# Performance work log

Hardware: AMD Instinct MI355X
Metric: run time of the kernel (lower is better)

Reference implementation:

```python
import jax, jax.numpy as jnp
import numpy as np

B, N, ND = 32, 512, 8        # batch, graph_size, node_dim
L, H, D = 4, 8, 512          # layers, heads, embed_dim
DK = D // H                  # key_dim = val_dim = 64
F = 2048                     # feed_forward_hidden
EPS = 1e-5


def setup_inputs() -> dict:
    key = jax.random.key(0)
    ks = jax.random.split(key, 16)
    u = lambda k, shape, s: jax.random.uniform(k, shape, jnp.float32, -s, s)
    x = jax.random.normal(ks[0], (B, N, ND), dtype=jnp.float32)
    mask = jax.random.randint(ks[1], (B, N, N), 0, 2).astype(jnp.int32)  # 1 = masked
    return {
        "x": x,
        "mask": mask,
        # init_embed Linear(node_dim, embed_dim)
        "We": u(ks[2], (ND, D), 1.0 / np.sqrt(ND)),
        "be": u(ks[3], (D,), 1.0 / np.sqrt(ND)),
        # per-head projections, stacked over layers; torch init: uniform(-1/sqrt(last_dim), ...)
        "Wq": u(ks[4], (L, H, D, DK), 1.0 / np.sqrt(DK)),
        "Wk": u(ks[5], (L, H, D, DK), 1.0 / np.sqrt(DK)),
        "Wv": u(ks[6], (L, H, D, DK), 1.0 / np.sqrt(DK)),
        "Wo": u(ks[7], (L, H, DK, D), 1.0 / np.sqrt(D)),
        # BatchNorm1d affine params (torch default: weight=1, bias=0)
        "g1": jnp.ones((L, D), jnp.float32), "bt1": jnp.zeros((L, D), jnp.float32),
        "g2": jnp.ones((L, D), jnp.float32), "bt2": jnp.zeros((L, D), jnp.float32),
        # FFN
        "W1": u(ks[8], (L, D, F), 1.0 / np.sqrt(D)),
        "bf1": u(ks[9], (L, F), 1.0 / np.sqrt(D)),
        "W2": u(ks[10], (L, F, D), 1.0 / np.sqrt(F)),
        "bf2": u(ks[11], (L, D), 1.0 / np.sqrt(F)),
    }


def _batch_norm(h, g, b):
    # BatchNorm1d in training mode over flattened (B*N, D), biased variance
    hf = h.reshape(-1, h.shape[-1])
    mu = hf.mean(axis=0)
    var = hf.var(axis=0)
    return (h - mu) * jax.lax.rsqrt(var + EPS) * g + b


def reference(x, mask, We, be, Wq, Wk, Wv, Wo, g1, bt1, W1, bf1, W2, bf2, g2, bt2):
    m = mask.astype(bool)[None]                      # [1,B,N,N], True = masked
    scale = 1.0 / np.sqrt(Wq.shape[-1])
    h = x @ We + be                                  # [B,N,D]
    for l in range(Wq.shape[0]):
        # hand-rolled per-head MHA (q = h, self-attention)
        Q = jnp.einsum('bnd,hdk->hbnk', h, Wq[l])
        K = jnp.einsum('bnd,hdk->hbnk', h, Wk[l])
        V = jnp.einsum('bnd,hdv->hbnv', h, Wv[l])
        scores = jnp.einsum('hbqk,hbnk->hbqn', Q, K) * scale   # [H,B,N,N]
        scores = jnp.where(m, -jnp.inf, scores)
        attn = jax.nn.softmax(scores, axis=-1)
        attn = jnp.where(m, 0.0, attn)               # second mask-zeroing pass
        heads = jnp.einsum('hbqn,hbnv->hbqv', attn, V)
        out = jnp.einsum('hbqv,hvd->bqd', heads, Wo[l])
        h = _batch_norm(h + out, g1[l], bt1[l])      # residual + BN
        ff = jax.nn.relu(h @ W1[l] + bf1[l]) @ W2[l] + bf2[l]
        h = _batch_norm(h + ff, g2[l], bt2[l])       # residual + BN
    return (h, h.mean(axis=1))
```

## Files before the change

### kernel.cpp

```cpp
#include <hip/hip_runtime.h>
#include <hip/hip_fp16.h>
#include <math.h>

#define BN_ROWS 16384
#define DIM 512
#define FF 2048
#define LAYERS 4
#define NSEQ 512
#define BATCH 32

typedef _Float16 f16;
typedef __attribute__((ext_vector_type(8))) _Float16 f16x8;
typedef __attribute__((ext_vector_type(4))) _Float16 f16x4;
typedef __attribute__((ext_vector_type(4))) float f32x4;
typedef unsigned long long u64;

__device__ __forceinline__ f32x4 mfma_f16(f16x8 a, f16x8 b, f32x4 c) {
    return __builtin_amdgcn_mfma_f32_16x16x32_f16(a, b, c, 0, 0, 0);
}
__device__ __forceinline__ void gload_lds16(const f16* g, f16* l) {
    __builtin_amdgcn_global_load_lds(
        (const __attribute__((address_space(1))) unsigned int*)g,
        (__attribute__((address_space(3))) unsigned int*)l, 16, 0, 0);
}

__global__ __launch_bounds__(256)
void pack_qkv(const float* __restrict__ Wq, const float* __restrict__ Wk,
              const float* __restrict__ Wv, f16* __restrict__ oh) {
    size_t i = (size_t)blockIdx.x * 256 + threadIdx.x;
    int d = i & 511;
    size_t rr = i >> 9;
    int row = (int)(rr % 1536);
    int lay = (int)(rr / 1536);
    int which = row >> 9, hh = (row >> 6) & 7, k = row & 63;
    const float* W = which == 0 ? Wq : which == 1 ? Wk : Wv;
    oh[i] = (f16)W[(((size_t)lay * 8 + hh) * 512 + d) * 64 + k];
}

__global__ __launch_bounds__(256)
void transpose_w(const float* __restrict__ in, f16* __restrict__ oh, int R, int C) {
    size_t i = (size_t)blockIdx.x * 256 + threadIdx.x;
    int r = (int)(i % R);
    size_t t = i / R;
    int c = (int)(t % C);
    int lay = (int)(t / C);
    oh[i] = (f16)in[((size_t)lay * R + r) * C + c];
}

__global__ __launch_bounds__(256)
void pack_mask(const int* __restrict__ mask, u64* __restrict__ pm) {
    int wid = (blockIdx.x * 256 + threadIdx.x) >> 6;
    int lane = threadIdx.x & 63;
    for (int i = 0; i < 64; i++) {
        size_t word = (size_t)wid * 64 + i;
        u64 bal = __ballot(mask[word * 64 + lane] != 0);
        if (lane == 0) pm[word] = bal;
    }
}

__global__ __launch_bounds__(512)
void embed_kernel(const float* __restrict__ x, const float* __restrict__ We,
                  const float* __restrict__ be, float* __restrict__ h,
                  f16* __restrict__ hf) {
    int row = blockIdx.x, d = threadIdx.x;
    const float* xr = x + (size_t)row * 8;
    float acc = be[d];
#pragma unroll
    for (int c = 0; c < 8; c++) acc += xr[c] * We[c * DIM + d];
    size_t idx = (size_t)row * DIM + d;
    h[idx] = acc;
    hf[idx] = (f16)acc;
}

template<int OUT>
__global__ __launch_bounds__(256)
void gemm_f16(const f16* __restrict__ A, const f16* __restrict__ Bt,
              const float* __restrict__ bias,
              void* __restrict__ O0, void* __restrict__ O1, void* __restrict__ O2,
              int M, int N, int K) {
    __shared__ f16 As[4096];
    __shared__ f16 Bs[4096];
    const int gx = gridDim.x;
    const int nwg = gx * gridDim.y;
    const int id = blockIdx.y * gx + blockIdx.x;
    const int chunk = nwg >> 3;
    const int sid = (id & 7) * chunk + (id >> 3);
    const int row0 = (sid / gx) * 128, col0 = (sid % gx) * 128;

    const int tid = threadIdx.x, l = tid & 63, w = tid >> 6;
    const int wr = w >> 1, wc = w & 1;
    const int fr = l & 15, fq = l >> 4;
    const int srow = l >> 2, skg = (l & 3) * 8;

    f32x4 acc[4][4] = {};
    const size_t aoff = (size_t)(row0 + w * 32 + srow) * K + skg;
    const size_t boff = (size_t)(col0 + w * 32 + srow) * K + skg;

    for (int k0 = 0; k0 < K; k0 += 32) {
        __syncthreads();
        gload_lds16(A + aoff + k0,           &As[(w * 2 + 0) * 512]);
        gload_lds16(A + aoff + 16 * K + k0,  &As[(w * 2 + 1) * 512]);
        gload_lds16(Bt + boff + k0,          &Bs[(w * 2 + 0) * 512]);
        gload_lds16(Bt + boff + 16 * K + k0, &Bs[(w * 2 + 1) * 512]);
        __syncthreads();
        f16x8 a[4], b[4];
#pragma unroll
        for (int i = 0; i < 4; i++)
            a[i] = *(const f16x8*)&As[(wr * 64 + i * 16 + fr) * 32 + fq * 8];
#pragma unroll
        for (int j = 0; j < 4; j++)
            b[j] = *(const f16x8*)&Bs[(wc * 64 + j * 16 + fr) * 32 + fq * 8];
#pragma unroll
        for (int i = 0; i < 4; i++)
#pragma unroll
            for (int j = 0; j < 4; j++)
                acc[i][j] = mfma_f16(a[i], b[j], acc[i][j]);
    }

    if (OUT == 1) {
        f16* C = (f16*)O0;
#pragma unroll
        for (int j = 0; j < 4; j++) {
            int gcol = col0 + wc * 64 + j * 16 + fr;
            float bv = bias[gcol];
#pragma unroll
            for (int i = 0; i < 4; i++) {
                int gr = row0 + wr * 64 + i * 16 + fq * 4;
#pragma unroll
                for (int r = 0; r < 4; r++)
                    C[(size_t)(gr + r) * N + gcol] = (f16)fmaxf(acc[i][j][r] + bv, 0.f);
            }
        }
    } else if (OUT == 2) {
        f16* Qo = (f16*)O0; f16* Ko = (f16*)O1; f16* Vo = (f16*)O2;
#pragma unroll
        for (int j = 0; j < 4; j++) {
            int gcol = col0 + wc * 64 + j * 16 + fr;
            if (gcol < 1024) {
                f16* dst = gcol < 512 ? Qo : Ko;
                int cc = gcol & 511;
#pragma unroll
                for (int i = 0; i < 4; i++) {
                    int gr = row0 + wr * 64 + i * 16 + fq * 4;
#pragma unroll
                    for (int r = 0; r < 4; r++)
                        dst[(size_t)(gr + r) * 512 + cc] = (f16)acc[i][j][r];
                }
            } else {
                int hh = (gcol - 1024) >> 6, v = gcol & 63;
#pragma unroll
                for (int i = 0; i < 4; i++) {
                    int gr = row0 + wr * 64 + i * 16 + fq * 4;
                    int b = gr >> 9, n = gr & 511;
                    f16x4 sv;
#pragma unroll
                    for (int r = 0; r < 4; r++) sv[r] = (f16)acc[i][j][r];
                    *(f16x4*)&Vo[(((size_t)b * 8 + hh) * 64 + v) * 512 + n] = sv;
                }
            }
        }
    } else {
        float* hres = (float*)O0;
        float* st   = (float*)O1;
#pragma unroll
        for (int j = 0; j < 4; j++) {
            int gcol = col0 + wc * 64 + j * 16 + fr;
            float bv = bias ? bias[gcol] : 0.f;
            float csum = 0.f, csq = 0.f;
#pragma unroll
            for (int i = 0; i < 4; i++) {
                int gr = row0 + wr * 64 + i * 16 + fq * 4;
#pragma unroll
                for (int r = 0; r < 4; r++) {
                    size_t idx = (size_t)(gr + r) * N + gcol;
                    float v = acc[i][j][r] + bv + hres[idx];
                    hres[idx] = v;
                    csum += v; csq += v * v;
                }
            }
            csum += __shfl_down(csum, 32, 64); csum += __shfl_down(csum, 16, 64);
            csq  += __shfl_down(csq,  32, 64); csq  += __shfl_down(csq,  16, 64);
            if (fq == 0) {
                atomicAdd(&st[gcol], csum);
                atomicAdd(&st[gcol + 512], csq);
            }
        }
    }
}

__global__ __launch_bounds__(256)
void attn_flash(const f16* __restrict__ Q, const f16* __restrict__ Kg,
                const f16* __restrict__ Vt, const u64* __restrict__ pmask,
                f16* __restrict__ attf) {
    int id = blockIdx.x;
    int wgid = (id & 7) * 128 + (id >> 3);
    int qc = wgid & 3;
    int gid = wgid >> 2;
    int b = gid & 31, hd = gid >> 5;

    __shared__ f16 Kl[2][4096];
    __shared__ f16 Vl[2][4096];
    __shared__ f16 Plds[4][1024];

    const int tid = threadIdx.x, w = tid >> 6, l = tid & 63;
    const int fr = l & 15, fq = l >> 4;

    const int brow = qc * 128 + w * 32;
    const size_t qbase = ((size_t)b * NSEQ + brow) * DIM + hd * 64;
    f16x8 qa[2][2];
#pragma unroll
    for (int sub = 0; sub < 2; sub++)
#pragma unroll
        for (int ks = 0; ks < 2; ks++)
            qa[sub][ks] = *(const f16x8*)(Q + qbase + (size_t)(sub * 16 + fr) * DIM + ks * 32 + fq * 8);

    const f16* ksrc = Kg + (size_t)b * NSEQ * DIM + hd * 64;
    const f16* vsrc = Vt + ((size_t)b * 8 + hd) * 64 * 512;
    const u64* mrow = pmask + ((size_t)b * NSEQ + brow) * 8;

    const int sr = tid & 63;
    const int sg0 = tid >> 6;
    const int sg1 = sg0 + 4;

    const float SC = 0.18033688011112042f;
    const float THR = 11.0f;

    float mu[2][4];
    f32x4 O[2][4] = {};
    f32x4 S1[2] = {};
#pragma unroll
    for (int s = 0; s < 2; s++)
#pragma unroll
        for (int r = 0; r < 4; r++) mu[s][r] = -1e30f;

    f16x8 vones;
#pragma unroll
    for (int i = 0; i < 8; i++) vones[i] = (f16)1.0f;

    char* Pb = (char*)&Plds[w][0];

    gload_lds16(ksrc + (size_t)sr * DIM + sg0 * 8, &Kl[0][tid * 8]);
    gload_lds16(ksrc + (size_t)sr * DIM + sg1 * 8, &Kl[0][2048 + tid * 8]);
    gload_lds16(vsrc + (size_t)sr * 512 + sg0 * 8, &Vl[0][tid * 8]);
    gload_lds16(vsrc + (size_t)sr * 512 + sg1 * 8, &Vl[0][2048 + tid * 8]);

    for (int c = 0; c < 8; c++) {
        const int buf = c & 1;
        __syncthreads();
        if (c < 7) {
            const int n1 = (c + 1) * 64;
            gload_lds16(ksrc + (size_t)(n1 + sr) * DIM + sg0 * 8, &Kl[buf ^ 1][tid * 8]);
            gload_lds16(ksrc + (size_t)(n1 + sr) * DIM + sg1 * 8, &Kl[buf ^ 1][2048 + tid * 8]);
            gload_lds16(vsrc + (size_t)sr * 512 + n1 + sg0 * 8,   &Vl[buf ^ 1][tid * 8]);
            gload_lds16(vsrc + (size_t)sr * 512 + n1 + sg1 * 8,   &Vl[buf ^ 1][2048 + tid * 8]);
        }

        f16x8 kb[4][2];
#pragma unroll
        for (int nt = 0; nt < 4; nt++)
#pragma unroll
            for (int ks = 0; ks < 2; ks++)
                kb[nt][ks] = *(const f16x8*)&Kl[buf][(ks * 4 + fq) * 512 + (nt * 16 + fr) * 8];

        f32x4 ps[2][4];
#pragma unroll
        for (int sub = 0; sub < 2; sub++)
#pragma unroll
            for (int nt = 0; nt < 4; nt++) {
                f32x4 a = {};
                a = mfma_f16(qa[sub][0], kb[nt][0], a);
                a = mfma_f16(qa[sub][1], kb[nt][1], a);
                ps[sub][nt] = a;
            }
#pragma unroll
        for (int sub = 0; sub < 2; sub++)
#pragma unroll
            for (int rr = 0; rr < 4; rr++) {
                u64 bits = mrow[(size_t)(sub * 16 + fq * 4 + rr) * 8 + c];
#pragma unroll
                for (int nt = 0; nt < 4; nt++) {
                    float u = ps[sub][nt][rr] * SC;
                    ps[sub][nt][rr] = ((bits >> (nt * 16 + fr)) & 1ull) ? -INFINITY : u;
                }
            }

        f16x8 vb[4][2];
#pragma unroll
        for (int vt = 0; vt < 4; vt++)
#pragma unroll
            for (int ks = 0; ks < 2; ks++)
                vb[vt][ks] = *(const f16x8*)&Vl[buf][(ks * 4 + fq) * 512 + (vt * 16 + fr) * 8];

#pragma unroll
        for (int sub = 0; sub < 2; sub++) {
            float lmax[4];
#pragma unroll
            for (int rr = 0; rr < 4; rr++)
                lmax[rr] = fmaxf(fmaxf(ps[sub][0][rr], ps[sub][1][rr]),
                                 fmaxf(ps[sub][2][rr], ps[sub][3][rr]));
            bool over = (lmax[0] > mu[sub][0] + THR) | (lmax[1] > mu[sub][1] + THR) |
                        (lmax[2] > mu[sub][2] + THR) | (lmax[3] > mu[sub][3] + THR);
            if (__any(over)) {
#pragma unroll
                for (int rr = 0; rr < 4; rr++) {
                    float v = lmax[rr];
#pragma unroll
                    for (int msk = 1; msk < 16; msk <<= 1)
                        v = fmaxf(v, __shfl_xor(v, msk, 64));
                    float mn = fmaxf(mu[sub][rr], v);
                    float sc = exp2f(mu[sub][rr] - mn);
                    mu[sub][rr] = mn;
                    S1[sub][rr] *= sc;
#pragma unroll
                    for (int vt = 0; vt < 4; vt++)
                        O[sub][vt][rr] *= sc;
                }
            }
#pragma unroll
            for (int nt = 0; nt < 4; nt++)
#pragma unroll
                for (int rr = 0; rr < 4; rr++)
                    ps[sub][nt][rr] = exp2f(ps[sub][nt][rr] - mu[sub][rr]);
#pragma unroll
            for (int nt = 0; nt < 4; nt++)
#pragma unroll
                for (int rr = 0; rr < 4; rr++) {
                    int row = fq * 4 + rr;
                    int byte = ((row * 64 + nt * 16 + fr) * 2) ^ ((row & 7) << 4);
                    *(f16*)(Pb + byte) = (f16)ps[sub][nt][rr];
                }
            f16x8 pa[2];
#pragma unroll
            for (int ks = 0; ks < 2; ks++) {
                int byte = ((fr * 64 + ks * 32 + fq * 8) * 2) ^ ((fr & 7) << 4);
                pa[ks] = *(const f16x8*)(Pb + byte);
            }
            S1[sub] = mfma_f16(pa[0], vones, S1[sub]);
            S1[sub] = mfma_f16(pa[1], vones, S1[sub]);
#pragma unroll
            for (int vt = 0; vt < 4; vt++) {
                O[sub][vt] = mfma_f16(pa[0], vb[vt][0], O[sub][vt]);
                O[sub][vt] = mfma_f16(pa[1], vb[vt][1], O[sub][vt]);
            }
        }
    }
#pragma unroll
    for (int sub = 0; sub < 2; sub++) {
        float inv[4];
#pragma unroll
        for (int rr = 0; rr < 4; rr++) inv[rr] = 1.f / S1[sub][rr];
#pragma unroll
        for (int vt = 0; vt < 4; vt++)
#pragma unroll
            for (int rr = 0; rr < 4; rr++) {
                float v = O[sub][vt][rr] * inv[rr];
                size_t idx = ((size_t)b * NSEQ + brow + sub * 16 + fq * 4 + rr) * DIM
                             + hd * 64 + vt * 16 + fr;
                attf[idx] = (f16)v;
            }
    }
}

__global__ __launch_bounds__(256)
void bn_apply(float* __restrict__ h, f16* __restrict__ hf,
              const float* __restrict__ sums, const float* __restrict__ g,
              const float* __restrict__ bt, float* __restrict__ outp) {
    size_t i4 = (size_t)blockIdx.x * 256 + threadIdx.x;
    size_t idx = i4 * 4;
    int c = (int)(idx & (DIM - 1));
    float4 hv = *(float4*)&h[idx];
    float4 s4 = *(const float4*)&sums[c];
    float4 q4 = *(const float4*)&sums[DIM + c];
    float4 g4 = *(const float4*)&g[c];
    float4 b4 = *(const float4*)&bt[c];
    float o[4];
    const float invn = 1.f / BN_ROWS;
#pragma unroll
    for (int j = 0; j < 4; j++) {
        float mu = ((const float*)&s4)[j] * invn;
        float var = ((const float*)&q4)[j] * invn - mu * mu;
        o[j] = (((const float*)&hv)[j] - mu) * rsqrtf(var + 1e-5f)
               * ((const float*)&g4)[j] + ((const float*)&b4)[j];
    }
    *(float4*)&h[idx] = *(float4*)o;
    if (outp) *(float4*)&outp[idx] = *(float4*)o;
    f16x4 s;
#pragma unroll
    for (int j = 0; j < 4; j++) s[j] = (f16)o[j];
    *(f16x4*)&hf[idx] = s;
}

__global__ __launch_bounds__(512)
void mean_kernel(const float* __restrict__ src, float* __restrict__ out2) {
    int b = blockIdx.x, seg = blockIdx.y, d = threadIdx.x;
    float acc = 0.f;
    for (int n = seg * 64; n < seg * 64 + 64; n++)
        acc += src[((size_t)b * NSEQ + n) * DIM + d];
    atomicAdd(&out2[b * DIM + d], acc * (1.f / NSEQ));
}

extern "C" void kernel_launch(void* const* d_in, const int* in_sizes, int n_in,
                              void* d_out, int out_size, void* d_ws, size_t ws_size,
                              hipStream_t stream) {
    const float* x   = (const float*)d_in[0];
    const int*   mask= (const int*)d_in[1];
    const float* We  = (const float*)d_in[2];
    const float* be  = (const float*)d_in[3];
    const float* Wq  = (const float*)d_in[4];
    const float* Wk  = (const float*)d_in[5];
    const float* Wv  = (const float*)d_in[6];
    const float* Wo  = (const float*)d_in[7];
    const float* g1  = (const float*)d_in[8];
    const float* bt1 = (const float*)d_in[9];
    const float* g2  = (const float*)d_in[10];
    const float* bt2 = (const float*)d_in[11];
    const float* W1  = (const float*)d_in[12];
    const float* bf1 = (const float*)d_in[13];
    const float* W2  = (const float*)d_in[14];
    const float* bf2 = (const float*)d_in[15];
    float* out = (float*)d_out;

    const size_t MiB = 1ull << 20;
    const size_t M1 = (size_t)BN_ROWS * DIM;
    char* base = (char*)d_ws;
    float* h     = (float*)base;
    f16*   hf    = (f16*)(base + 32 * MiB);
    f16*   Qf    = (f16*)(base + 48 * MiB);
    f16*   Kf    = (f16*)(base + 64 * MiB);
    f16*   Vt    = (f16*)(base + 80 * MiB);
    f16*   attf  = (f16*)(base + 96 * MiB);
    f16*   ffh   = (f16*)(base + 48 * MiB);
    float* stats = (float*)(base + 112 * MiB);
    u64*   pmask = (u64*)(base + 112 * MiB + 65536);
    f16*   wqkv  = (f16*)(base + 114 * MiB);
    f16*   wo    = wqkv + (size_t)4 * 1536 * 512;
    f16*   w1t   = wo   + (size_t)4 * 512 * 512;
    f16*   w2t   = w1t  + (size_t)4 * 2048 * 512;

    pack_qkv<<<dim3(4 * 1536 * 512 / 256), dim3(256), 0, stream>>>(Wq, Wk, Wv, wqkv);
    transpose_w<<<dim3(4 * 512 * 512 / 256), dim3(256), 0, stream>>>(Wo, wo, 512, 512);
    transpose_w<<<dim3(4 * 512 * 2048 / 256), dim3(256), 0, stream>>>(W1, w1t, 512, 2048);
    transpose_w<<<dim3(4 * 2048 * 512 / 256), dim3(256), 0, stream>>>(W2, w2t, 2048, 512);
    pack_mask<<<dim3(512), dim3(256), 0, stream>>>(mask, pmask);
    hipMemsetAsync(out + M1, 0, BATCH * DIM * sizeof(float), stream);

    embed_kernel<<<dim3(BN_ROWS), dim3(512), 0, stream>>>(x, We, be, h, hf);

    for (int l = 0; l < LAYERS; l++) {
        gemm_f16<2><<<dim3(1536 / 128, 128), dim3(256), 0, stream>>>(
            hf, wqkv + (size_t)l * 1536 * 512, nullptr, Qf, Kf, Vt,
            BN_ROWS, 1536, 512);

        attn_flash<<<dim3(1024), dim3(256), 0, stream>>>(Qf, Kf, Vt, pmask, attf);

        hipMemsetAsync(stats, 0, 1024 * sizeof(float), stream);
        gemm_f16<3><<<dim3(512 / 128, 128), dim3(256), 0, stream>>>(
            attf, wo + (size_t)l * 512 * 512, nullptr, h, stats, nullptr,
            BN_ROWS, 512, 512);
        bn_apply<<<dim3(M1 / 1024), dim3(256), 0, stream>>>(
            h, hf, stats, g1 + l * DIM, bt1 + l * DIM, nullptr);

        hipMemsetAsync(stats, 0, 1024 * sizeof(float), stream);
        gemm_f16<1><<<dim3(FF / 128, BN_ROWS / 128), dim3(256), 0, stream>>>(
            hf, w1t + (size_t)l * FF * DIM, bf1 + (size_t)l * FF,
            ffh, nullptr, nullptr, BN_ROWS, FF, DIM);
        gemm_f16<3><<<dim3(DIM / 128, BN_ROWS / 128), dim3(256), 0, stream>>>(
            ffh, w2t + (size_t)l * DIM * FF, bf2 + (size_t)l * DIM,
            h, stats, nullptr, BN_ROWS, DIM, FF);

        float* outp = (l == LAYERS - 1) ? out : nullptr;
        bn_apply<<<dim3(M1 / 1024), dim3(256), 0, stream>>>(
            h, hf, stats, g2 + l * DIM, bt2 + l * DIM, outp);
    }

    mean_kernel<<<dim3(BATCH, 8), dim3(512), 0, stream>>>(out, out + M1);
}
```

Measured before the change: 1.260 ms.

## Double-buffer LDS tiles in f16 GEMM to overlap global loads with MFMA

Splits the GEMM's shared-memory A/B tiles into two buffers and prefetches the next K-tile with global_load_lds while MFMAs run on the current one. This removes one of the two barriers per K step and hides global-load latency behind compute. The cost is double the LDS per block, which may lower occupancy. The overlap only happens if the compiler does not insert a full vmcnt wait before the LDS reads.

```diff
diff --git a/kernel.cpp b/kernel.cpp
--- a/kernel.cpp
+++ b/kernel.cpp
@@ -78,8 +78,8 @@
               const float* __restrict__ bias,
               void* __restrict__ O0, void* __restrict__ O1, void* __restrict__ O2,
               int M, int N, int K) {
-    __shared__ f16 As[4096];
-    __shared__ f16 Bs[4096];
+    __shared__ f16 As[2][4096];
+    __shared__ f16 Bs[2][4096];
     const int gx = gridDim.x;
     const int nwg = gx * gridDim.y;
     const int id = blockIdx.y * gx + blockIdx.x;
@@ -93,23 +93,33 @@
     const int srow = l >> 2, skg = (l & 3) * 8;
 
     f32x4 acc[4][4] = {};
-    const size_t aoff = (size_t)(row0 + w * 32 + srow) * K + skg;
-    const size_t boff = (size_t)(col0 + w * 32 + srow) * K + skg;
-
-    for (int k0 = 0; k0 < K; k0 += 32) {
+    const f16* Ab = A + (size_t)(row0 + w * 32 + srow) * K + skg;
+    const f16* Bb = Bt + (size_t)(col0 + w * 32 + srow) * K + skg;
+    const size_t a16 = (size_t)16 * K;
+    const int nt = K >> 5;
+
+    gload_lds16(Ab,       &As[0][(w * 2 + 0) * 512]);
+    gload_lds16(Ab + a16, &As[0][(w * 2 + 1) * 512]);
+    gload_lds16(Bb,       &Bs[0][(w * 2 + 0) * 512]);
+    gload_lds16(Bb + a16, &Bs[0][(w * 2 + 1) * 512]);
+
+    for (int kt = 0; kt < nt; kt++) {
+        const int buf = kt & 1;
         __syncthreads();
-        gload_lds16(A + aoff + k0,           &As[(w * 2 + 0) * 512]);
-        gload_lds16(A + aoff + 16 * K + k0,  &As[(w * 2 + 1) * 512]);
-        gload_lds16(Bt + boff + k0,          &Bs[(w * 2 + 0) * 512]);
-        gload_lds16(Bt + boff + 16 * K + k0, &Bs[(w * 2 + 1) * 512]);
-        __syncthreads();
+        if (kt + 1 < nt) {
+            const int k0 = (kt + 1) * 32;
+            gload_lds16(Ab + k0,       &As[buf ^ 1][(w * 2 + 0) * 512]);
+            gload_lds16(Ab + a16 + k0, &As[buf ^ 1][(w * 2 + 1) * 512]);
+            gload_lds16(Bb + k0,       &Bs[buf ^ 1][(w * 2 + 0) * 512]);
+            gload_lds16(Bb + a16 + k0, &Bs[buf ^ 1][(w * 2 + 1) * 512]);
+        }
         f16x8 a[4], b[4];
 #pragma unroll
         for (int i = 0; i < 4; i++)
-            a[i] = *(const f16x8*)&As[(wr * 64 + i * 16 + fr) * 32 + fq * 8];
+            a[i] = *(const f16x8*)&As[buf][(wr * 64 + i * 16 + fr) * 32 + fq * 8];
 #pragma unroll
         for (int j = 0; j < 4; j++)
-            b[j] = *(const f16x8*)&Bs[(wc * 64 + j * 16 + fr) * 32 + fq * 8];
+            b[j] = *(const f16x8*)&Bs[buf][(wc * 64 + j * 16 + fr) * 32 + fq * 8];
 #pragma unroll
         for (int i = 0; i < 4; i++)
 #pragma unroll
```

Result: faster. 1.224 ms (-2.9%).
